# Kernel tuning notes

Hardware: AMD Instinct MI355X
Metric: run time of the kernel (lower is better)

The kernel has to match this reference:

```python
import jax, jax.numpy as jnp
import numpy as np

R, C, E, H = 64, 2048, 128, 8  # num_rows(cells), num_cols(genes), embed_dim, heads
HD = E // H

def setup_inputs() -> dict:
    key = jax.random.key(0)
    ks = jax.random.split(key, 7)
    s = 1.0 / np.sqrt(E)
    return {
        "x": jax.random.normal(ks[0], (R, C, E), dtype=jnp.float32),
        "Wq": jax.random.normal(ks[1], (E, E), dtype=jnp.float32) * s,
        "bq": jax.random.normal(ks[2], (E,), dtype=jnp.float32) * 0.01,
        "Wk": jax.random.normal(ks[3], (E, E), dtype=jnp.float32) * s,
        "bk": jax.random.normal(ks[4], (E,), dtype=jnp.float32) * 0.01,
        "Wv": jax.random.normal(ks[5], (E, E), dtype=jnp.float32) * s,
        "bv": jax.random.normal(ks[6], (E,), dtype=jnp.float32) * 0.01,
    }

def reference(x, Wq, bq, Wk, bk, Wv, bv):
    num_rows, num_cols, embed_dim = x.shape
    head_dim = embed_dim // H

    def proj(W, b):
        # (R,C,E) -> (R,C,H,hd) -> (H,C,R,hd)
        y = (x @ W.T + b).reshape(num_rows, num_cols, H, head_dim)
        return jnp.transpose(y, (2, 1, 0, 3))

    q = proj(Wq, bq)
    k = proj(Wk, bk)
    v = proj(Wv, bv)

    # softmax over head_dim for q (before flattening rows into features)
    q = jax.nn.softmax(q, axis=-1).reshape(H, num_cols, num_rows * head_dim)
    k = k.reshape(H, num_cols, num_rows * head_dim)
    v = v.reshape(H, num_cols, num_rows * head_dim)

    dim = q.shape[-1]  # num_rows * head_dim
    k = jax.nn.softmax(k, axis=-2)      # softmax over sequence (num_cols)
    q = q * (dim ** -0.5)

    attn_weights = jnp.einsum('hnd,hmd->hnm', q, k)   # (H, C, C)
    context = jnp.einsum('hnd,hne->hde', k, v)        # (H, D, D)
    out = jnp.einsum('hnd,hde->hne', q, context)      # (H, C, D)

    out = out.reshape(H, num_cols, num_rows, head_dim)
    out = jnp.transpose(out, (2, 1, 0, 3)).reshape(num_rows, num_cols, embed_dim)
    return (out, attn_weights)
```

## Files before the change

### kernel.cpp

```cpp
#include <hip/hip_runtime.h>
#include <hip/hip_bf16.h>
#include <stdint.h>

typedef unsigned short u16;
typedef __attribute__((ext_vector_type(8))) short s16x8;
typedef __attribute__((ext_vector_type(4))) float f32x4;

__device__ __forceinline__ u16 f2bf(float f) {
    union { float f; uint32_t u; } v; v.f = f;
    uint32_t r = v.u + 0x7fffu + ((v.u >> 16) & 1u);
    return (u16)(r >> 16);
}
__device__ __forceinline__ float bf2f(u16 b) {
    union { uint32_t u; float f; } v; v.u = ((uint32_t)b) << 16;
    return v.f;
}
__device__ __forceinline__ void split2(float f, u16& h, u16& l) {
    h = f2bf(f);
    l = f2bf(f - bf2f(h));
}

__device__ __forceinline__ void load_lds16(const void* g, void* l) {
    __builtin_amdgcn_global_load_lds(
        (const __attribute__((address_space(1))) unsigned int*)g,
        (__attribute__((address_space(3))) unsigned int*)l,
        16, 0, 0);
}

__global__ __launch_bounds__(256)
void wsplit_kernel(const float* __restrict__ Wq, const float* __restrict__ Wk,
                   const float* __restrict__ Wv, u16* __restrict__ Wsp)
{
    const int i = blockIdx.x * 256 + threadIdx.x;
    const int p = i >> 14;
    const int j = i & 16383;
    const float* W = (p == 0) ? Wq : (p == 1) ? Wk : Wv;
    const float v = W[j];
    u16 h, l; split2(v, h, l);
    Wsp[(size_t)p * 32768 + j]         = h;
    Wsp[(size_t)p * 32768 + 16384 + j] = l;
}

__global__ __launch_bounds__(256, 4)
void proj_kernel(const float* __restrict__ x, const u16* __restrict__ Wsp,
                 const float* __restrict__ bq, const float* __restrict__ bk,
                 const float* __restrict__ bv,
                 u16* __restrict__ Qs, float* __restrict__ KTf, u16* __restrict__ VT)
{
    __shared__ u16 Xh[64 * 132], Xl[64 * 132];
    const int tid = threadIdx.x;
    const int i0 = blockIdx.x * 64;
    const int r  = i0 >> 11;
    const int c0 = i0 & 2047;

    {
        const int col = (tid & 31) * 4;
        const int rb  = tid >> 5;
        #pragma unroll
        for (int pp = 0; pp < 8; ++pp) {
            int row = pp * 8 + rb;
            float4 v = *(const float4*)(x + (size_t)(i0 + row) * 128 + col);
            ushort4 hi, lo;
            split2(v.x, hi.x, lo.x); split2(v.y, hi.y, lo.y);
            split2(v.z, hi.z, lo.z); split2(v.w, hi.w, lo.w);
            *(ushort4*)&Xh[row * 132 + col] = hi;
            *(ushort4*)&Xl[row * 132 + col] = lo;
        }
    }
    __syncthreads();

    const int lane = tid & 63;
    const int w = tid >> 6;
    const int wr = w >> 1, wc = w & 1;
    const int lr = lane & 15, kc = lane >> 4;
    const f32x4 fzero = {0.f, 0.f, 0.f, 0.f};

    const float* const bp[3] = { bq, bk, bv };

    #pragma unroll
    for (int p = 0; p < 3; ++p) {
        const u16* Wh = Wsp + (size_t)p * 32768;

        f32x4 acc[2][4];
        #pragma unroll
        for (int m = 0; m < 2; ++m)
            #pragma unroll
            for (int n = 0; n < 4; ++n) acc[m][n] = fzero;

        #pragma unroll
        for (int k0 = 0; k0 < 128; k0 += 32) {
            s16x8 ah[2], al[2];
            #pragma unroll
            for (int m = 0; m < 2; ++m) {
                ah[m] = *(const s16x8*)&Xh[(wr*32 + m*16 + lr) * 132 + k0 + kc*8];
                al[m] = *(const s16x8*)&Xl[(wr*32 + m*16 + lr) * 132 + k0 + kc*8];
            }
            #pragma unroll
            for (int n = 0; n < 4; ++n) {
                const u16* wb = Wh + (wc*64 + n*16 + lr) * 128 + k0 + kc*8;
                s16x8 bh = *(const s16x8*)wb;
                s16x8 bl = *(const s16x8*)(wb + 16384);
                #pragma unroll
                for (int m = 0; m < 2; ++m) {
                    acc[m][n] = __builtin_amdgcn_mfma_f32_16x16x32_bf16(ah[m], bh, acc[m][n], 0, 0, 0);
                    acc[m][n] = __builtin_amdgcn_mfma_f32_16x16x32_bf16(al[m], bh, acc[m][n], 0, 0, 0);
                    acc[m][n] = __builtin_amdgcn_mfma_f32_16x16x32_bf16(ah[m], bl, acc[m][n], 0, 0, 0);
                }
            }
        }

        float bvals[4];
        #pragma unroll
        for (int n = 0; n < 4; ++n) bvals[n] = bp[p][wc*64 + n*16 + lr];

        if (p == 0) {
            #pragma unroll
            for (int m = 0; m < 2; ++m) {
                #pragma unroll
                for (int n = 0; n < 4; ++n) {
                    const int h  = wc*4 + n;
                    const int cb = c0 + wr*32 + m*16 + kc*4;
                    #pragma unroll
                    for (int j = 0; j < 4; ++j) {
                        float v = acc[m][n][j] + bvals[n];
                        float mx = v;
                        #pragma unroll
                        for (int s = 8; s >= 1; s >>= 1)
                            mx = fmaxf(mx, __shfl_xor(mx, s, 16));
                        float e = __expf(v - mx);
                        float sm = e;
                        #pragma unroll
                        for (int s = 8; s >= 1; s >>= 1)
                            sm += __shfl_xor(sm, s, 16);
                        float o = e / sm * 0.03125f;
                        Qs[((size_t)h * 2048 + cb + j) * 1024 + r*16 + lr] = f2bf(o);
                    }
                }
            }
        } else if (p == 1) {
            #pragma unroll
            for (int m = 0; m < 2; ++m) {
                #pragma unroll
                for (int n = 0; n < 4; ++n) {
                    const int h  = wc*4 + n;
                    const int cb = c0 + wr*32 + m*16 + kc*4;
                    float4 pk;
                    pk.x = acc[m][n][0] + bvals[n];
                    pk.y = acc[m][n][1] + bvals[n];
                    pk.z = acc[m][n][2] + bvals[n];
                    pk.w = acc[m][n][3] + bvals[n];
                    *(float4*)&KTf[((size_t)(h*1024 + r*16 + lr)) * 2048 + cb] = pk;
                }
            }
        } else {
            #pragma unroll
            for (int m = 0; m < 2; ++m) {
                #pragma unroll
                for (int n = 0; n < 4; ++n) {
                    const int h  = wc*4 + n;
                    const int cb = c0 + wr*32 + m*16 + kc*4;
                    ushort4 pk;
                    pk.x = f2bf(acc[m][n][0] + bvals[n]);
                    pk.y = f2bf(acc[m][n][1] + bvals[n]);
                    pk.z = f2bf(acc[m][n][2] + bvals[n]);
                    pk.w = f2bf(acc[m][n][3] + bvals[n]);
                    *(ushort4*)&VT[((size_t)(h*1024 + r*16 + lr)) * 2048 + cb] = pk;
                }
            }
        }
    }
}

__global__ __launch_bounds__(256)
void ksm_kernel(const float* __restrict__ KTf, u16* __restrict__ KTsm)
{
    const float* p = KTf + (size_t)blockIdx.x * 2048;
    u16* o = KTsm + (size_t)blockIdx.x * 2048;
    const int t = threadIdx.x;
    float4 a = *(const float4*)(p + t * 8);
    float4 b = *(const float4*)(p + t * 8 + 4);
    float v[8] = {a.x, a.y, a.z, a.w, b.x, b.y, b.z, b.w};
    float mx = v[0];
    #pragma unroll
    for (int j = 1; j < 8; ++j) mx = fmaxf(mx, v[j]);
    #pragma unroll
    for (int s = 32; s >= 1; s >>= 1) mx = fmaxf(mx, __shfl_xor(mx, s, 64));
    __shared__ float redm[4], reds[4];
    const int w = t >> 6;
    if ((t & 63) == 0) redm[w] = mx;
    __syncthreads();
    mx = fmaxf(fmaxf(redm[0], redm[1]), fmaxf(redm[2], redm[3]));
    float e[8]; float sm = 0.f;
    #pragma unroll
    for (int j = 0; j < 8; ++j) { e[j] = __expf(v[j] - mx); sm += e[j]; }
    #pragma unroll
    for (int s = 32; s >= 1; s >>= 1) sm += __shfl_xor(sm, s, 64);
    if ((t & 63) == 0) reds[w] = sm;
    __syncthreads();
    sm = reds[0] + reds[1] + reds[2] + reds[3];
    const float inv = 1.f / sm;
    uint4 ov; u16* op = (u16*)&ov;
    #pragma unroll
    for (int j = 0; j < 8; ++j) op[j] = f2bf(e[j] * inv);
    *(uint4*)(o + t * 8) = ov;
}

__global__ __launch_bounds__(256)
void ktrans_kernel(const u16* __restrict__ KTsm, u16* __restrict__ Ksm)
{
    const int h  = blockIdx.z;
    const int d0 = blockIdx.y * 64;
    const int c0 = blockIdx.x * 64;
    __shared__ u16 tile[64][72];
    const int t = threadIdx.x;
    #pragma unroll
    for (int i = 0; i < 2; ++i) {
        int g = t + i * 256;
        int dr = g >> 3;
        int cc = (g & 7) * 8;
        uint4 val = *(const uint4*)(KTsm + ((size_t)(h * 1024 + d0 + dr)) * 2048 + c0 + cc);
        *(uint4*)&tile[dr][cc] = val;
    }
    __syncthreads();
    #pragma unroll
    for (int i = 0; i < 2; ++i) {
        int g = t + i * 256;
        int cr = g >> 3;
        int dc = (g & 7) * 8;
        uint4 ov; u16* op = (u16*)&ov;
        #pragma unroll
        for (int j = 0; j < 8; ++j) op[j] = tile[dc + j][cr];
        *(uint4*)(Ksm + ((size_t)(h * 2048 + c0 + cr)) * 1024 + d0 + dc) = ov;
    }
}

template<int MODE>
__global__ __launch_bounds__(256, 2)
void gemm_bt(const u16* __restrict__ Aall, const u16* __restrict__ Ball,
             float* __restrict__ outF, u16* __restrict__ outB,
             const int M, const int N, const int K)
{
    const int gx = gridDim.x, gy = gridDim.y;
    const int perh = gx * gy;
    int flat = blockIdx.x + gx * (blockIdx.y + gy * blockIdx.z);
    flat = (flat & 7) * perh + (flat >> 3);
    const int h   = flat / perh;
    const int rem = flat - h * perh;
    const int m0  = (rem / gx) * 128;
    const int n0  = (rem % gx) * 128;
    const u16* A = Aall + (size_t)h * M * K;
    const u16* B = Ball + (size_t)h * N * K;
    __shared__ u16 As[128 * 64];
    __shared__ u16 Bs[128 * 64];
    const int tid = threadIdx.x;
    const int lane = tid & 63;
    const int w = tid >> 6;
    const int wr = w >> 1, wc = w & 1;
    const int lr = lane & 15, kc = lane >> 4;
    const f32x4 fzero = {0.f, 0.f, 0.f, 0.f};

    f32x4 acc[4][4];
    #pragma unroll
    for (int m = 0; m < 4; ++m)
        #pragma unroll
        for (int n = 0; n < 4; ++n) acc[m][n] = fzero;

    const int srow = tid >> 3;
    const int scol = (tid & 7) * 8;
    const u16* ga = A + (size_t)(m0 + srow) * K + scol;
    const u16* gb = B + (size_t)(n0 + srow) * K + scol;
    char* lA = (char*)As + tid * 16;
    char* lB = (char*)Bs + tid * 16;
    const size_t rstep = (size_t)32 * K;

    for (int k0 = 0; k0 < K; k0 += 64) {
        __syncthreads();
        load_lds16(ga,             lA);
        load_lds16(ga +     rstep, lA + 4096);
        load_lds16(ga + 2 * rstep, lA + 8192);
        load_lds16(ga + 3 * rstep, lA + 12288);
        load_lds16(gb,             lB);
        load_lds16(gb +     rstep, lB + 4096);
        load_lds16(gb + 2 * rstep, lB + 8192);
        load_lds16(gb + 3 * rstep, lB + 12288);
        ga += 64; gb += 64;
        __syncthreads();

        #pragma unroll
        for (int kk = 0; kk < 64; kk += 32) {
            s16x8 a[4], b[4];
            #pragma unroll
            for (int m = 0; m < 4; ++m)
                a[m] = *(const s16x8*)((const char*)As + (((wr*64 + m*16 + lr) * 64) + kk + kc*8) * 2);
            #pragma unroll
            for (int n = 0; n < 4; ++n)
                b[n] = *(const s16x8*)((const char*)Bs + (((wc*64 + n*16 + lr) * 64) + kk + kc*8) * 2);
            #pragma unroll
            for (int m = 0; m < 4; ++m)
                #pragma unroll
                for (int n = 0; n < 4; ++n)
                    acc[m][n] = __builtin_amdgcn_mfma_f32_16x16x32_bf16(a[m], b[n], acc[m][n], 0, 0, 0);
        }
    }

    #pragma unroll
    for (int m = 0; m < 4; ++m) {
        #pragma unroll
        for (int n = 0; n < 4; ++n) {
            const int grow0 = m0 + wr*64 + m*16 + kc*4;
            const int gcol  = n0 + wc*64 + n*16 + lr;
            #pragma unroll
            for (int j = 0; j < 4; ++j) {
                const float v = acc[m][n][j];
                const int grow = grow0 + j;
                if (MODE == 0) {
                    __builtin_nontemporal_store(v, &outF[(size_t)h * M * N + (size_t)grow * N + gcol]);
                } else if (MODE == 1) {
                    outB[(size_t)h * M * N + (size_t)grow * N + gcol] = f2bf(v);
                } else {
                    const int rr = gcol >> 4, hd = gcol & 15;
                    __builtin_nontemporal_store(v, &outF[((size_t)rr * 2048 + grow) * 128 + h * 16 + hd]);
                }
            }
        }
    }
}

extern "C" void kernel_launch(void* const* d_in, const int* in_sizes, int n_in,
                              void* d_out, int out_size, void* d_ws, size_t ws_size,
                              hipStream_t stream)
{
    const float* x  = (const float*)d_in[0];
    const float* Wq = (const float*)d_in[1];
    const float* bq = (const float*)d_in[2];
    const float* Wk = (const float*)d_in[3];
    const float* bk = (const float*)d_in[4];
    const float* Wv = (const float*)d_in[5];
    const float* bv = (const float*)d_in[6];

    float* outT = (float*)d_out;
    float* attn = outT + (size_t)64 * 2048 * 128;

    u16* Qs   = (u16*)d_ws;
    u16* Ksm  = Qs + (size_t)8 * 2048 * 1024;
    u16* KTsm = (u16*)outT;
    u16*   VT  = (u16*)attn;
    u16*   CT  = VT + (size_t)8 * 1024 * 2048;
    float* KTf = (float*)(CT + (size_t)8 * 1024 * 1024);
    u16*   Wsp = (u16*)(KTf + (size_t)8 * 1024 * 2048);

    wsplit_kernel<<<192, 256, 0, stream>>>(Wq, Wk, Wv, Wsp);
    proj_kernel<<<2048, 256, 0, stream>>>(x, Wsp, bq, bk, bv, Qs, KTf, VT);
    ksm_kernel<<<8192, 256, 0, stream>>>(KTf, KTsm);
    ktrans_kernel<<<dim3(32, 16, 8), 256, 0, stream>>>(KTsm, Ksm);
    gemm_bt<1><<<dim3(8, 8, 8),  256, 0, stream>>>(VT, KTsm, nullptr, CT, 1024, 1024, 2048);
    gemm_bt<2><<<dim3(8, 16, 8), 256, 0, stream>>>(Qs, CT, outT, nullptr, 2048, 1024, 1024);
    gemm_bt<0><<<dim3(16, 16, 8), 256, 0, stream>>>(Qs, Ksm, attn, nullptr, 2048, 2048, 1024);
}
```

Baseline: 542.2 us.

## Stage split weights through double-buffered LDS with async global-to-LDS loads

Reorganizes the pre-split bf16 hi/lo weight buffer into padded 32-wide K-slices (row stride 40) and streams each slice into a double-buffered LDS region with global_load_lds, prefetching the next slice while MFMAs consume the current one. This replaces per-wave direct global loads of the weight fragments and also pads the X tiles to a 136 stride to cut bank conflicts. The cost is extra LDS per block (launch bounds lowered to 2 blocks/SM) and a __syncthreads per K-slice.

```diff
diff --git a/kernel.cpp b/kernel.cpp
--- a/kernel.cpp
+++ b/kernel.cpp
@@ -32,26 +32,40 @@
                    const float* __restrict__ Wv, u16* __restrict__ Wsp)
 {
     const int i = blockIdx.x * 256 + threadIdx.x;
-    const int p = i >> 14;
-    const int j = i & 16383;
+    const int p  = i >> 14;
+    const int r  = i & 16383;
+    const int s  = r >> 12;
+    const int r2 = r & 4095;
+    const int e  = r2 >> 5;
+    const int kk = r2 & 31;
     const float* W = (p == 0) ? Wq : (p == 1) ? Wk : Wv;
-    const float v = W[j];
+    const float v = W[e * 128 + s * 32 + kk];
     u16 h, l; split2(v, h, l);
-    Wsp[(size_t)p * 32768 + j]         = h;
-    Wsp[(size_t)p * 32768 + 16384 + j] = l;
-}
-
-__global__ __launch_bounds__(256, 4)
+    const size_t base = (size_t)(p * 4 + s) * 10240;
+    Wsp[base + e * 40 + kk]        = h;
+    Wsp[base + 5120 + e * 40 + kk] = l;
+}
+
+__global__ __launch_bounds__(256, 2)
 void proj_kernel(const float* __restrict__ x, const u16* __restrict__ Wsp,
                  const float* __restrict__ bq, const float* __restrict__ bk,
                  const float* __restrict__ bv,
                  u16* __restrict__ Qs, float* __restrict__ KTf, u16* __restrict__ VT)
 {
-    __shared__ u16 Xh[64 * 132], Xl[64 * 132];
+    __shared__ __align__(16) u16 Xh[64 * 136], Xl[64 * 136];
+    __shared__ __align__(16) u16 Wlds[2][10240];
     const int tid = threadIdx.x;
     const int i0 = blockIdx.x * 64;
     const int r  = i0 >> 11;
     const int c0 = i0 & 2047;
+
+    {
+        const char* wsrc = (const char*)Wsp;
+        char* wdst = (char*)&Wlds[0][0];
+        #pragma unroll
+        for (int i = 0; i < 5; ++i)
+            load_lds16(wsrc + i * 4096 + tid * 16, wdst + i * 4096 + tid * 16);
+    }
 
     {
         const int col = (tid & 31) * 4;
@@ -63,8 +77,8 @@
             ushort4 hi, lo;
             split2(v.x, hi.x, lo.x); split2(v.y, hi.y, lo.y);
             split2(v.z, hi.z, lo.z); split2(v.w, hi.w, lo.w);
-            *(ushort4*)&Xh[row * 132 + col] = hi;
-            *(ushort4*)&Xl[row * 132 + col] = lo;
+            *(ushort4*)&Xh[row * 136 + col] = hi;
+            *(ushort4*)&Xl[row * 136 + col] = lo;
         }
     }
     __syncthreads();
@@ -79,8 +93,6 @@
 
     #pragma unroll
     for (int p = 0; p < 3; ++p) {
-        const u16* Wh = Wsp + (size_t)p * 32768;
-
         f32x4 acc[2][4];
         #pragma unroll
         for (int m = 0; m < 2; ++m)
@@ -88,18 +100,28 @@
             for (int n = 0; n < 4; ++n) acc[m][n] = fzero;
 
         #pragma unroll
-        for (int k0 = 0; k0 < 128; k0 += 32) {
+        for (int s = 0; s < 4; ++s) {
+            const int idx = p * 4 + s;
+            if (idx < 11) {
+                const char* wsrc = (const char*)Wsp + (size_t)(idx + 1) * 20480;
+                char* wdst = (char*)&Wlds[(idx + 1) & 1][0];
+                #pragma unroll
+                for (int i = 0; i < 5; ++i)
+                    load_lds16(wsrc + i * 4096 + tid * 16, wdst + i * 4096 + tid * 16);
+            }
+
+            const u16* wbuf = Wlds[idx & 1];
             s16x8 ah[2], al[2];
             #pragma unroll
             for (int m = 0; m < 2; ++m) {
-                ah[m] = *(const s16x8*)&Xh[(wr*32 + m*16 + lr) * 132 + k0 + kc*8];
-                al[m] = *(const s16x8*)&Xl[(wr*32 + m*16 + lr) * 132 + k0 + kc*8];
+                ah[m] = *(const s16x8*)&Xh[(wr*32 + m*16 + lr) * 136 + s*32 + kc*8];
+                al[m] = *(const s16x8*)&Xl[(wr*32 + m*16 + lr) * 136 + s*32 + kc*8];
             }
             #pragma unroll
             for (int n = 0; n < 4; ++n) {
-                const u16* wb = Wh + (wc*64 + n*16 + lr) * 128 + k0 + kc*8;
-                s16x8 bh = *(const s16x8*)wb;
-                s16x8 bl = *(const s16x8*)(wb + 16384);
+                const u16* wrow = wbuf + (wc*64 + n*16 + lr) * 40 + kc*8;
+                s16x8 bh = *(const s16x8*)wrow;
+                s16x8 bl = *(const s16x8*)(wrow + 5120);
                 #pragma unroll
                 for (int m = 0; m < 2; ++m) {
                     acc[m][n] = __builtin_amdgcn_mfma_f32_16x16x32_bf16(ah[m], bh, acc[m][n], 0, 0, 0);
@@ -107,6 +129,7 @@
                     acc[m][n] = __builtin_amdgcn_mfma_f32_16x16x32_bf16(ah[m], bl, acc[m][n], 0, 0, 0);
                 }
             }
+            __syncthreads();
         }
 
         float bvals[4];
```

Result: faster. 504.5 us (-7.0%).
